# Optimization experiments

Measured on AMD Instinct MI355X. Metric: run time of the kernel, lower is better.

## Reference

```python
import jax, jax.numpy as jnp
import numpy as np

L, H, Wn, C = 2048, 768, 1024, 64


def setup_inputs() -> dict:
    key = jax.random.key(0)
    ks = jax.random.split(key, 12)
    s = 1.0 / np.sqrt(H)
    s3 = 1.0 / np.sqrt(3 * H)
    return {
        "tok_embs": jax.random.normal(ks[0], (L, H), jnp.float32),
        "wmask": jax.random.randint(ks[1], (L,), 0, Wn + 1),  # 1-indexed word positions, 0 = ignore
        "text_length": Wn,
        "label_embs": jax.random.normal(ks[2], (C, H), jnp.float32),
        "W_tok": jax.random.normal(ks[3], (H, 2 * H), jnp.float32) * s,
        "b_tok": jnp.zeros((2 * H,), jnp.float32),
        "W_lab": jax.random.normal(ks[4], (H, 2 * H), jnp.float32) * s,
        "b_lab": jnp.zeros((2 * H,), jnp.float32),
        "W1": jax.random.normal(ks[5], (3 * H, H), jnp.float32) * s3,
        "b1": jnp.zeros((H,), jnp.float32),
        "W2": jax.random.normal(ks[6], (H, 3), jnp.float32) * s,
        "b2": jnp.zeros((3,), jnp.float32),
    }


def reference(tok_embs, wmask, text_length, label_embs, W_tok, b_tok, W_lab, b_lab, W1, b1, W2, b2):
    Wd = text_length
    Hd = tok_embs.shape[-1]
    # --- word-level scatter pooling: we[wmask-1] = tok_embs where wmask > 0 ---
    # route masked-out tokens to a dummy row Wd, then drop it (jit-safe, no nonzero)
    tgt = jnp.where(wmask > 0, wmask - 1, Wd)
    we = jnp.zeros((Wd + 1, Hd), tok_embs.dtype).at[tgt].set(tok_embs)[:Wd]  # (W, H)
    # --- scorer ---
    t = (we @ W_tok + b_tok).reshape(Wd, 2, Hd)        # (W, 2, H)
    lb = (label_embs @ W_lab + b_lab).reshape(-1, 2, Hd)  # (C, 2, H)
    Cd = lb.shape[0]
    t0 = jnp.broadcast_to(t[:, None, 0, :], (Wd, Cd, Hd))
    l0 = jnp.broadcast_to(lb[None, :, 0, :], (Wd, Cd, Hd))
    prod = t[:, None, 1, :] * lb[None, :, 1, :]        # (W, C, H)
    cat = jnp.concatenate([t0, l0, prod], axis=-1)     # (W, C, 3H)
    h = jax.nn.relu(cat @ W1 + b1)                     # (W, C, H)
    scores = h @ W2 + b2                               # (W, C, 3)
    return scores
```

## Files before the change

kernel.cpp:

```cpp
#include <hip/hip_runtime.h>
#include <hip/hip_bf16.h>

static constexpr int Hd = 768;
static constexpr int H2 = 1536;
static constexpr int Cn = 64;

typedef __attribute__((ext_vector_type(8))) short short8;
typedef __attribute__((ext_vector_type(4))) float f32x4;
typedef unsigned short us;

__device__ inline unsigned int f2bf2(float a, float b) {
    __hip_bfloat162 h = __float22bfloat162_rn(float2{a, b});
    return *reinterpret_cast<unsigned int*>(&h);
}

__device__ inline void split1(float x, us& h, us& l) {
    __hip_bfloat16 hb = __float2bfloat16(x);
    float hf = __bfloat162float(hb);
    __hip_bfloat16 lb_ = __float2bfloat16(x - hf);
    h = *reinterpret_cast<us*>(&hb);
    l = *reinterpret_cast<us*>(&lb_);
}

__device__ inline us f2b(float x) {
    __hip_bfloat16 b = __float2bfloat16(x);
    return *reinterpret_cast<us*>(&b);
}

__device__ inline float b2f(us u) {
    __hip_bfloat16 b = *reinterpret_cast<__hip_bfloat16*>(&u);
    return __bfloat162float(b);
}

__device__ inline short8 bfmul8(short8 a, short8 b) {
    short8 r;
#pragma unroll
    for (int e = 0; e < 8; e += 2) {
        unsigned int p = f2bf2(b2f((us)a[e]) * b2f((us)b[e]),
                               b2f((us)a[e + 1]) * b2f((us)b[e + 1]));
        r[e] = (short)(p & 0xffff);
        r[e + 1] = (short)(p >> 16);
    }
    return r;
}

__device__ inline int swz(int row, int q) {
    return row * 32 + ((q ^ ((row >> 1) & 3)) << 3);
}

__device__ inline void gload16(const void* g, void* l) {
    __builtin_amdgcn_global_load_lds(
        (const __attribute__((address_space(1))) unsigned int*)g,
        (__attribute__((address_space(3))) unsigned int*)l, 16, 0, 0);
}

__global__ void k_init(int* widx, int Wd) {
    int i = blockIdx.x * 256 + threadIdx.x;
    if (i < Wd) widx[i] = -1;
}

__global__ void k_scatter(const int* __restrict__ wmask, int* widx, int L, int Wd) {
    int i = blockIdx.x * 256 + threadIdx.x;
    if (i < L) {
        int m = wmask[i];
        if (m > 0 && m <= Wd) atomicMax(&widx[m - 1], i);
    }
}

__global__ void k_build_we_split(const float4* __restrict__ tok, const int* __restrict__ widx,
                                 us* __restrict__ weh, us* __restrict__ wel, int Wd) {
    int i = blockIdx.x * 256 + threadIdx.x;
    if (i >= Wd * 192) return;
    int w = i / 192, c4 = i - w * 192;
    int idx = widx[w];
    float4 v = (idx >= 0) ? tok[idx * 192 + c4] : float4{0.f, 0.f, 0.f, 0.f};
    us hh[4], ll[4];
    split1(v.x, hh[0], ll[0]);
    split1(v.y, hh[1], ll[1]);
    split1(v.z, hh[2], ll[2]);
    split1(v.w, hh[3], ll[3]);
    size_t o = (size_t)w * Hd + c4 * 4;
    *(ushort4*)&weh[o] = ushort4{hh[0], hh[1], hh[2], hh[3]};
    *(ushort4*)&wel[o] = ushort4{ll[0], ll[1], ll[2], ll[3]};
}

struct TSArgs {
    const float* src[5];
    us* th[5];
    us* tl[5];
    int ld[5];
    int N[5];
};
__global__ __launch_bounds__(256)
void k_tsplit(TSArgs a) {
    __shared__ float tile[64][65];
    const int z = blockIdx.z;
    const int n0 = blockIdx.x * 64, k0 = blockIdx.y * 64;
    if (n0 >= a.N[z]) return;
    const float* W = a.src[z];
    const int ld = a.ld[z];
    for (int idx = threadIdx.x; idx < 4096; idx += 256) {
        int kk = idx >> 6, nn = idx & 63;
        tile[kk][nn] = W[(size_t)(k0 + kk) * ld + n0 + nn];
    }
    __syncthreads();
    us* Th = a.th[z];
    us* Tl = a.tl[z];
    for (int idx = threadIdx.x; idx < 4096; idx += 256) {
        int nn = idx >> 6, kk = idx & 63;
        us h, l;
        split1(tile[kk][nn], h, l);
        size_t o = (size_t)(n0 + nn) * Hd + k0 + kk;
        Th[o] = h;
        Tl[o] = l;
    }
}

__global__ __launch_bounds__(256)
void k_split(const float* __restrict__ x, int lda, int cols,
             us* __restrict__ h, us* __restrict__ l, int n4) {
    int i = blockIdx.x * 256 + threadIdx.x;
    if (i >= n4) return;
    int c4 = cols >> 2;
    int row = i / c4, cc = (i - row * c4) * 4;
    float4 v = *(const float4*)&x[(size_t)row * lda + cc];
    us hh[4], ll[4];
    split1(v.x, hh[0], ll[0]);
    split1(v.y, hh[1], ll[1]);
    split1(v.z, hh[2], ll[2]);
    split1(v.w, hh[3], ll[3]);
    size_t o = (size_t)row * cols + cc;
    *(ushort4*)&h[o] = ushort4{hh[0], hh[1], hh[2], hh[3]};
    *(ushort4*)&l[o] = ushort4{ll[0], ll[1], ll[2], ll[3]};
}

__global__ __launch_bounds__(256)
void k_gemm2(const us* __restrict__ Ah, const us* __restrict__ Al,
             const us* __restrict__ BhT, const us* __restrict__ BlT,
             float* __restrict__ Cpart, int M, int N, int K) {
    __shared__ __align__(16) us S[2][4][64 * 32];
    const int tid = threadIdx.x, wave = tid >> 6, lane = tid & 63;
    const int quad = lane >> 4, l15 = lane & 15;
    const int wm = wave & 1, wn = wave >> 1;
    const int m0 = blockIdx.y * 64, n0 = blockIdx.x * 64;
    const int Ks = K / gridDim.z, kbeg = blockIdx.z * Ks, kend = kbeg + Ks;
    float* C = Cpart + (size_t)blockIdx.z * M * N;

    const int srow = wave * 16 + (lane >> 2), soff = (lane & 3) * 8;
    const size_t gaB = (size_t)(m0 + srow) * K + soff;
    const size_t gbB = (size_t)(n0 + srow) * K + soff;
    const int lo = wave * 16 * 32;

    f32x4 acc[2][2];
#pragma unroll
    for (int a = 0; a < 2; ++a)
#pragma unroll
        for (int b = 0; b < 2; ++b) acc[a][b] = (f32x4){0.f, 0.f, 0.f, 0.f};

    auto stage = [&](int p, int k0) {
        gload16(Ah + gaB + k0, &S[p][0][lo]);
        gload16(Al + gaB + k0, &S[p][1][lo]);
        gload16(BhT + gbB + k0, &S[p][2][lo]);
        gload16(BlT + gbB + k0, &S[p][3][lo]);
    };

    int p = 0;
    stage(0, kbeg);
    for (int k0 = kbeg; k0 < kend; k0 += 32) {
        __syncthreads();
        if (k0 + 32 < kend) stage(p ^ 1, k0 + 32);
        short8 ah[2], al[2], bh[2], bl[2];
#pragma unroll
        for (int mt = 0; mt < 2; ++mt) {
            int off = (wm * 32 + mt * 16 + l15) * 32 + quad * 8;
            ah[mt] = *(const short8*)&S[p][0][off];
            al[mt] = *(const short8*)&S[p][1][off];
        }
#pragma unroll
        for (int nt = 0; nt < 2; ++nt) {
            int off = (wn * 32 + nt * 16 + l15) * 32 + quad * 8;
            bh[nt] = *(const short8*)&S[p][2][off];
            bl[nt] = *(const short8*)&S[p][3][off];
        }
#pragma unroll
        for (int mt = 0; mt < 2; ++mt)
#pragma unroll
            for (int nt = 0; nt < 2; ++nt) {
                acc[mt][nt] = __builtin_amdgcn_mfma_f32_16x16x32_bf16(al[mt], bh[nt], acc[mt][nt], 0, 0, 0);
                acc[mt][nt] = __builtin_amdgcn_mfma_f32_16x16x32_bf16(ah[mt], bl[nt], acc[mt][nt], 0, 0, 0);
                acc[mt][nt] = __builtin_amdgcn_mfma_f32_16x16x32_bf16(ah[mt], bh[nt], acc[mt][nt], 0, 0, 0);
            }
        p ^= 1;
    }
#pragma unroll
    for (int mt = 0; mt < 2; ++mt)
#pragma unroll
        for (int nt = 0; nt < 2; ++nt) {
            int col = n0 + wn * 32 + nt * 16 + l15;
#pragma unroll
            for (int reg = 0; reg < 4; ++reg) {
                int row = m0 + wm * 32 + mt * 16 + quad * 4 + reg;
                C[(size_t)row * N + col] = acc[mt][nt][reg];
            }
        }
}

__global__ __launch_bounds__(256)
void k_gemm3(const us* __restrict__ Ah, const us* __restrict__ Al,
             const us* __restrict__ BhT, const us* __restrict__ BlT,
             const float* __restrict__ bias, float* __restrict__ outF,
             us* __restrict__ sh, us* __restrict__ sl, us* __restrict__ bh16,
             int scols, int N, int K) {
    __shared__ __align__(16) us S[2][4][64 * 32];
    const int tid = threadIdx.x, wave = tid >> 6, lane = tid & 63;
    const int quad = lane >> 4, l15 = lane & 15;
    const int wm = wave & 1, wn = wave >> 1;
    const int m0 = blockIdx.y * 64, n0 = blockIdx.x * 64;

    const int srow = wave * 16 + (lane >> 2), soff = (lane & 3) * 8;
    const size_t gaB = (size_t)(m0 + srow) * K + soff;
    const size_t gbB = (size_t)(n0 + srow) * K + soff;
    const int lo = wave * 16 * 32;

    f32x4 acc[2][2];
#pragma unroll
    for (int a = 0; a < 2; ++a)
#pragma unroll
        for (int b = 0; b < 2; ++b) acc[a][b] = (f32x4){0.f, 0.f, 0.f, 0.f};

    auto stage = [&](int p, int k0) {
        gload16(Ah + gaB + k0, &S[p][0][lo]);
        gload16(Al + gaB + k0, &S[p][1][lo]);
        gload16(BhT + gbB + k0, &S[p][2][lo]);
        gload16(BlT + gbB + k0, &S[p][3][lo]);
    };

    int p = 0;
    stage(0, 0);
    for (int k0 = 0; k0 < K; k0 += 32) {
        __syncthreads();
        if (k0 + 32 < K) stage(p ^ 1, k0 + 32);
        short8 ah[2], al[2], bh[2], bl[2];
#pragma unroll
        for (int mt = 0; mt < 2; ++mt) {
            int off = (wm * 32 + mt * 16 + l15) * 32 + quad * 8;
            ah[mt] = *(const short8*)&S[p][0][off];
            al[mt] = *(const short8*)&S[p][1][off];
        }
#pragma unroll
        for (int nt = 0; nt < 2; ++nt) {
            int off = (wn * 32 + nt * 16 + l15) * 32 + quad * 8;
            bh[nt] = *(const short8*)&S[p][2][off];
            bl[nt] = *(const short8*)&S[p][3][off];
        }
#pragma unroll
        for (int mt = 0; mt < 2; ++mt)
#pragma unroll
            for (int nt = 0; nt < 2; ++nt) {
                acc[mt][nt] = __builtin_amdgcn_mfma_f32_16x16x32_bf16(al[mt], bh[nt], acc[mt][nt], 0, 0, 0);
                acc[mt][nt] = __builtin_amdgcn_mfma_f32_16x16x32_bf16(ah[mt], bl[nt], acc[mt][nt], 0, 0, 0);
                acc[mt][nt] = __builtin_amdgcn_mfma_f32_16x16x32_bf16(ah[mt], bh[nt], acc[mt][nt], 0, 0, 0);
            }
        p ^= 1;
    }
#pragma unroll
    for (int mt = 0; mt < 2; ++mt)
#pragma unroll
        for (int nt = 0; nt < 2; ++nt) {
            int col = n0 + wn * 32 + nt * 16 + l15;
            float bb = bias ? bias[col] : 0.f;
#pragma unroll
            for (int reg = 0; reg < 4; ++reg) {
                int row = m0 + wm * 32 + mt * 16 + quad * 4 + reg;
                float v = acc[mt][nt][reg] + bb;
                if (outF) outF[(size_t)row * N + col] = v;
                if (sh) {
                    if (col < scols) {
                        us h, l;
                        split1(v, h, l);
                        size_t o = (size_t)row * scols + col;
                        sh[o] = h;
                        sl[o] = l;
                    } else if (bh16) {
                        bh16[(size_t)row * scols + (col - scols)] = f2b(v);
                    }
                }
            }
        }
}

__global__ __launch_bounds__(256)
void k_reduce(const float* __restrict__ part, int S, int MN, int N,
              const float* __restrict__ bias, float* __restrict__ outF,
              us* __restrict__ sh, us* __restrict__ sl, int scols,
              us* __restrict__ bh16) {
    int i = blockIdx.x * 256 + threadIdx.x;
    if (i >= MN) return;
    float v = 0.f;
    for (int s = 0; s < S; ++s) v += part[(size_t)s * MN + i];
    int row = i / N, col = i - row * N;
    if (bias) v += bias[col];
    if (outF) outF[i] = v;
    if (col < scols) {
        if (sh) {
            us h, l;
            split1(v, h, l);
            size_t o = (size_t)row * scols + col;
            sh[o] = h;
            sl[o] = l;
        }
    } else if (bh16) {
        bh16[(size_t)row * scols + (col - scols)] = f2b(v);
    }
}

__global__ __launch_bounds__(256, 3)
void k_mfma7(const us* __restrict__ t1b,
             const us* __restrict__ W1ct,
             const us* __restrict__ lb1b,
             const float* __restrict__ Aw,
             const float* __restrict__ Bc,
             const float* __restrict__ W2,
             float* __restrict__ scr) {
    __shared__ __align__(16) us As[2][128 * 32];
    __shared__ __align__(16) us Bs[2][128 * 32];
    __shared__ float sred[128 * 3];

    const int tid = threadIdx.x, wave = tid >> 6, lane = tid & 63;
    const int quad = lane >> 4, l15 = lane & 15;
    const int wm = wave & 1, wn = wave >> 1;

    const int b = blockIdx.x;
    const int xcd = b & 7, slot = b >> 3;
    const int cgrp = slot / 48, tt = slot % 48;
    const int my = tt / 6, jx = tt - my * 6;
    const int c = cgrp * 8 + xcd;
    const int jt = jx * 128, m0 = my * 128;

    for (int i = tid; i < 128 * 3; i += 256) sred[i] = 0.f;

    const int aro = tid >> 1;
    const int qb = (tid & 1) * 2;
    const int kbase = qb * 8;
    const us* gA = W1ct + (size_t)(jt + aro) * Hd + kbase;
    const us* gL = lb1b + (size_t)c * Hd + kbase;
    const us* gB = t1b + (size_t)(m0 + aro) * Hd + kbase;
    const int w0 = swz(aro, qb), w1 = swz(aro, qb + 1);

    f32x4 acc[4][4];
#pragma unroll
    for (int mt = 0; mt < 4; ++mt)
#pragma unroll
        for (int nt = 0; nt < 4; ++nt) acc[mt][nt] = (f32x4){0.f, 0.f, 0.f, 0.f};

    short8 aw0l, aw0h, al0l, al0h, b0l, b0h;
    short8 aw1l, aw1h, al1l, al1h, b1l, b1h;

    aw0l = *(const short8*)(gA + 0);  aw0h = *(const short8*)(gA + 8);
    al0l = *(const short8*)(gL + 0);  al0h = *(const short8*)(gL + 8);
    b0l  = *(const short8*)(gB + 0);  b0h  = *(const short8*)(gB + 8);
    aw1l = *(const short8*)(gA + 32); aw1h = *(const short8*)(gA + 40);
    al1l = *(const short8*)(gL + 32); al1h = *(const short8*)(gL + 40);
    b1l  = *(const short8*)(gB + 32); b1h  = *(const short8*)(gB + 40);
    *(short8*)&As[0][w0] = bfmul8(aw0l, al0l);
    *(short8*)&As[0][w1] = bfmul8(aw0h, al0h);
    *(short8*)&Bs[0][w0] = b0l;
    *(short8*)&Bs[0][w1] = b0h;
    __syncthreads();

    for (int k = 0; k < Hd; k += 64) {
        {
            short8 af[4], bf[4];
#pragma unroll
            for (int mt = 0; mt < 4; ++mt)
                af[mt] = *(const short8*)&As[0][swz(wm * 64 + mt * 16 + l15, quad)];
#pragma unroll
            for (int nt = 0; nt < 4; ++nt)
                bf[nt] = *(const short8*)&Bs[0][swz(wn * 64 + nt * 16 + l15, quad)];
            if (k + 64 < Hd) {
                aw0l = *(const short8*)(gA + k + 64); aw0h = *(const short8*)(gA + k + 72);
                al0l = *(const short8*)(gL + k + 64); al0h = *(const short8*)(gL + k + 72);
                b0l  = *(const short8*)(gB + k + 64); b0h  = *(const short8*)(gB + k + 72);
            }
#pragma unroll
            for (int mt = 0; mt < 4; ++mt)
#pragma unroll
                for (int nt = 0; nt < 4; ++nt)
                    acc[mt][nt] = __builtin_amdgcn_mfma_f32_16x16x32_bf16(
                        af[mt], bf[nt], acc[mt][nt], 0, 0, 0);
            *(short8*)&As[1][w0] = bfmul8(aw1l, al1l);
            *(short8*)&As[1][w1] = bfmul8(aw1h, al1h);
            *(short8*)&Bs[1][w0] = b1l;
            *(short8*)&Bs[1][w1] = b1h;
            __syncthreads();
        }
        {
            short8 af[4], bf[4];
#pragma unroll
            for (int mt = 0; mt < 4; ++mt)
                af[mt] = *(const short8*)&As[1][swz(wm * 64 + mt * 16 + l15, quad)];
#pragma unroll
            for (int nt = 0; nt < 4; ++nt)
                bf[nt] = *(const short8*)&Bs[1][swz(wn * 64 + nt * 16 + l15, quad)];
            if (k + 96 < Hd) {
                aw1l = *(const short8*)(gA + k + 96); aw1h = *(const short8*)(gA + k + 104);
                al1l = *(const short8*)(gL + k + 96); al1h = *(const short8*)(gL + k + 104);
                b1l  = *(const short8*)(gB + k + 96); b1h  = *(const short8*)(gB + k + 104);
            }
#pragma unroll
            for (int mt = 0; mt < 4; ++mt)
#pragma unroll
                for (int nt = 0; nt < 4; ++nt)
                    acc[mt][nt] = __builtin_amdgcn_mfma_f32_16x16x32_bf16(
                        af[mt], bf[nt], acc[mt][nt], 0, 0, 0);
            if (k + 64 < Hd) {
                *(short8*)&As[0][w0] = bfmul8(aw0l, al0l);
                *(short8*)&As[0][w1] = bfmul8(aw0h, al0h);
                *(short8*)&Bs[0][w0] = b0l;
                *(short8*)&Bs[0][w1] = b0h;
                __syncthreads();
            }
        }
    }

    float bcv[4][4], w2v[4][4][3];
#pragma unroll
    for (int mt = 0; mt < 4; ++mt) {
        const int jb = jt + wm * 64 + mt * 16 + quad * 4;
        float4 b4 = *(const float4*)&Bc[(size_t)c * Hd + jb];
        bcv[mt][0] = b4.x; bcv[mt][1] = b4.y; bcv[mt][2] = b4.z; bcv[mt][3] = b4.w;
#pragma unroll
        for (int reg = 0; reg < 4; ++reg)
#pragma unroll
            for (int r = 0; r < 3; ++r) w2v[mt][reg][r] = W2[(jb + reg) * 3 + r];
    }
#pragma unroll
    for (int nt = 0; nt < 4; ++nt) {
        const int w = m0 + wn * 64 + nt * 16 + l15;
        const float* awp = Aw + (size_t)w * Hd + jt + wm * 64;
        float s0 = 0.f, s1 = 0.f, s2 = 0.f;
#pragma unroll
        for (int mt = 0; mt < 4; ++mt) {
            float4 a4 = *(const float4*)&awp[mt * 16 + quad * 4];
            float av[4] = {a4.x, a4.y, a4.z, a4.w};
#pragma unroll
            for (int reg = 0; reg < 4; ++reg) {
                float h = acc[mt][nt][reg] + av[reg] + bcv[mt][reg];
                h = h > 0.f ? h : 0.f;
                s0 += h * w2v[mt][reg][0];
                s1 += h * w2v[mt][reg][1];
                s2 += h * w2v[mt][reg][2];
            }
        }
        s0 += __shfl_xor(s0, 16); s0 += __shfl_xor(s0, 32);
        s1 += __shfl_xor(s1, 16); s1 += __shfl_xor(s1, 32);
        s2 += __shfl_xor(s2, 16); s2 += __shfl_xor(s2, 32);
        if (quad == 0) {
            const int wl = wn * 64 + nt * 16 + l15;
            atomicAdd(&sred[wl * 3 + 0], s0);
            atomicAdd(&sred[wl * 3 + 1], s1);
            atomicAdd(&sred[wl * 3 + 2], s2);
        }
    }
    __syncthreads();
    float* slab = scr + ((size_t)jx * 1024 * Cn + (size_t)m0 * Cn + c) * 3;
    for (int i = tid; i < 128 * 3; i += 256) {
        int wl = i / 3, r = i - wl * 3;
        slab[(size_t)wl * Cn * 3 + r] = sred[i];
    }
}

__global__ __launch_bounds__(256)
void k_scores(const float* __restrict__ scr, const float* __restrict__ b2,
              float* __restrict__ out, int n) {
    int i = blockIdx.x * 256 + threadIdx.x;
    if (i >= n) return;
    float v = b2[i % 3];
#pragma unroll
    for (int s = 0; s < 6; ++s) v += scr[(size_t)s * n + i];
    out[i] = v;
}

extern "C" void kernel_launch(void* const* d_in, const int* in_sizes, int n_in,
                              void* d_out, int out_size, void* d_ws, size_t ws_size,
                              hipStream_t stream) {
    const float* tok    = (const float*)d_in[0];
    const int*   wmask  = (const int*)d_in[1];
    const float* labe   = (const float*)d_in[3];
    const float* W_tok  = (const float*)d_in[4];
    const float* b_tok  = (const float*)d_in[5];
    const float* W_lab  = (const float*)d_in[6];
    const float* b_lab  = (const float*)d_in[7];
    const float* W1     = (const float*)d_in[8];
    const float* b1     = (const float*)d_in[9];
    const float* W2     = (const float*)d_in[10];
    const float* b2     = (const float*)d_in[11];
    float* out = (float*)d_out;

    const int L  = in_sizes[1];
    const int Wd = out_size / (Cn * 3);

    char* ws = (char*)d_ws;
    size_t off = 0;
    auto alloc = [&](size_t bytes) { char* p = ws + off; off += (bytes + 255) & ~(size_t)255; return p; };
    int*   widx  = (int*)alloc(4096);
    float* Abuf  = (float*)alloc((size_t)Wd * Hd * 4);
    float* Bbuf  = (float*)alloc((size_t)Cn * Hd * 4);
    us* W1ct  = (us*)alloc((size_t)Hd * Hd * 2);
    us* W1cl  = (us*)alloc((size_t)Hd * Hd * 2);
    us* t1b   = (us*)alloc((size_t)Wd * Hd * 2);
    us* lb1b  = (us*)alloc((size_t)Cn * Hd * 2);
    float* scr = (float*)alloc((size_t)6 * Wd * Cn * 3 * 4);
    us* WtTh  = (us*)alloc((size_t)H2 * Hd * 2);
    us* WtTl  = (us*)alloc((size_t)H2 * Hd * 2);
    us* WlTh  = (us*)alloc((size_t)H2 * Hd * 2);
    us* WlTl  = (us*)alloc((size_t)H2 * Hd * 2);
    us* W1aTh = (us*)alloc((size_t)Hd * Hd * 2);
    us* W1aTl = (us*)alloc((size_t)Hd * Hd * 2);
    us* W1bTh = (us*)alloc((size_t)Hd * Hd * 2);
    us* W1bTl = (us*)alloc((size_t)Hd * Hd * 2);
    us* weh   = (us*)alloc((size_t)Wd * Hd * 2);
    us* wel   = (us*)alloc((size_t)Wd * Hd * 2);
    us* lah   = (us*)alloc((size_t)Cn * Hd * 2);
    us* lal   = (us*)alloc((size_t)Cn * Hd * 2);
    us* t0h   = (us*)alloc((size_t)Wd * Hd * 2);
    us* t0l   = (us*)alloc((size_t)Wd * Hd * 2);
    us* lb0h  = (us*)alloc((size_t)Cn * Hd * 2);
    us* lb0l  = (us*)alloc((size_t)Cn * Hd * 2);
    float* part = (float*)alloc((size_t)8 * Cn * H2 * 4);

    k_init<<<(Wd + 255) / 256, 256, 0, stream>>>(widx, Wd);
    k_scatter<<<(L + 255) / 256, 256, 0, stream>>>(wmask, widx, L, Wd);
    k_build_we_split<<<(Wd * 192 + 255) / 256, 256, 0, stream>>>((const float4*)tok, widx, weh, wel, Wd);

    TSArgs ts;
    ts.src[0] = W_tok;  ts.th[0] = WtTh;  ts.tl[0] = WtTl;  ts.ld[0] = H2; ts.N[0] = H2;
    ts.src[1] = W_lab;  ts.th[1] = WlTh;  ts.tl[1] = WlTl;  ts.ld[1] = H2; ts.N[1] = H2;
    ts.src[2] = W1;                         ts.th[2] = W1aTh; ts.tl[2] = W1aTl; ts.ld[2] = Hd; ts.N[2] = Hd;
    ts.src[3] = W1 + (size_t)Hd * Hd;       ts.th[3] = W1bTh; ts.tl[3] = W1bTl; ts.ld[3] = Hd; ts.N[3] = Hd;
    ts.src[4] = W1 + (size_t)2 * Hd * Hd;   ts.th[4] = W1ct;  ts.tl[4] = W1cl;  ts.ld[4] = Hd; ts.N[4] = Hd;
    k_tsplit<<<dim3(H2 / 64, Hd / 64, 5), 256, 0, stream>>>(ts);

    k_split<<<(Cn * Hd / 4 + 255) / 256, 256, 0, stream>>>(labe, Hd, Hd, lah, lal, Cn * Hd / 4);

    k_gemm3<<<dim3(H2 / 64, Wd / 64), 256, 0, stream>>>(weh, wel, WtTh, WtTl, b_tok,
                                                        nullptr, t0h, t0l, t1b, Hd, H2, Hd);

    k_gemm2<<<dim3(H2 / 64, 1, 8), 256, 0, stream>>>(lah, lal, WlTh, WlTl, part, Cn, H2, Hd);
    k_reduce<<<(Cn * H2 + 255) / 256, 256, 0, stream>>>(part, 8, Cn * H2, H2, b_lab, nullptr, lb0h, lb0l, Hd, lb1b);

    k_gemm3<<<dim3(Hd / 64, Wd / 64), 256, 0, stream>>>(t0h, t0l, W1aTh, W1aTl, nullptr,
                                                        Abuf, nullptr, nullptr, nullptr, 0, Hd, Hd);

    k_gemm2<<<dim3(Hd / 64, 1, 8), 256, 0, stream>>>(lb0h, lb0l, W1bTh, W1bTl, part, Cn, Hd, Hd);
    k_reduce<<<(Cn * Hd + 255) / 256, 256, 0, stream>>>(part, 8, Cn * Hd, Hd, b1, Bbuf, nullptr, nullptr, Hd, nullptr);

    k_mfma7<<<3072, 256, 0, stream>>>(t1b, W1ct, lb1b, Abuf, Bbuf, W2, scr);

    k_scores<<<(Wd * Cn * 3 + 255) / 256, 256, 0, stream>>>(scr, b2, out, Wd * Cn * 3);
}
```

Measured before the change: 276.1 us.

## Double word tile to 256 and load B fragments directly from global into registers

The main MFMA kernel now covers 256 word rows per block instead of 128, doubling the accumulator tile to 4x8 per wave and halving the grid. The B operand (t1b) is no longer staged through shared memory. Each wave loads its MFMA fragments straight from global memory into registers and double-buffers them. This removes the LDS writes, reads and their share of the barriers, and reuses each A tile across twice as many words. In exchange, register pressure rises (occupancy bound lowered to 2), global loads become strided per row, and fewer blocks may hurt load balance.

```diff
diff --git a/kernel.cpp b/kernel.cpp
--- a/kernel.cpp
+++ b/kernel.cpp
@@ -314,8 +314,8 @@
     }
 }
 
-__global__ __launch_bounds__(256, 3)
-void k_mfma7(const us* __restrict__ t1b,
+__global__ __launch_bounds__(256, 2)
+void k_mfma8(const us* __restrict__ t1b,
              const us* __restrict__ W1ct,
              const us* __restrict__ lb1b,
              const float* __restrict__ Aw,
@@ -323,8 +323,7 @@
              const float* __restrict__ W2,
              float* __restrict__ scr) {
     __shared__ __align__(16) us As[2][128 * 32];
-    __shared__ __align__(16) us Bs[2][128 * 32];
-    __shared__ float sred[128 * 3];
+    __shared__ float sred[256 * 3];
 
     const int tid = threadIdx.x, wave = tid >> 6, lane = tid & 63;
     const int quad = lane >> 4, l15 = lane & 15;
@@ -332,92 +331,91 @@
 
     const int b = blockIdx.x;
     const int xcd = b & 7, slot = b >> 3;
-    const int cgrp = slot / 48, tt = slot % 48;
+    const int cgrp = slot / 24, tt = slot % 24;
     const int my = tt / 6, jx = tt - my * 6;
     const int c = cgrp * 8 + xcd;
-    const int jt = jx * 128, m0 = my * 128;
-
-    for (int i = tid; i < 128 * 3; i += 256) sred[i] = 0.f;
+    const int jt = jx * 128, m0 = my * 256;
+
+    for (int i = tid; i < 256 * 3; i += 256) sred[i] = 0.f;
 
     const int aro = tid >> 1;
     const int qb = (tid & 1) * 2;
     const int kbase = qb * 8;
     const us* gA = W1ct + (size_t)(jt + aro) * Hd + kbase;
     const us* gL = lb1b + (size_t)c * Hd + kbase;
-    const us* gB = t1b + (size_t)(m0 + aro) * Hd + kbase;
     const int w0 = swz(aro, qb), w1 = swz(aro, qb + 1);
 
-    f32x4 acc[4][4];
+    const us* gB = t1b + (size_t)(m0 + wn * 128 + l15) * Hd + quad * 8;
+
+    f32x4 acc[4][8];
 #pragma unroll
     for (int mt = 0; mt < 4; ++mt)
 #pragma unroll
-        for (int nt = 0; nt < 4; ++nt) acc[mt][nt] = (f32x4){0.f, 0.f, 0.f, 0.f};
-
-    short8 aw0l, aw0h, al0l, al0h, b0l, b0h;
-    short8 aw1l, aw1h, al1l, al1h, b1l, b1h;
+        for (int nt = 0; nt < 8; ++nt) acc[mt][nt] = (f32x4){0.f, 0.f, 0.f, 0.f};
+
+    short8 aw0l, aw0h, aw1l, aw1h, all_, alh_;
+    short8 bcur[8], bnxt[8];
 
     aw0l = *(const short8*)(gA + 0);  aw0h = *(const short8*)(gA + 8);
-    al0l = *(const short8*)(gL + 0);  al0h = *(const short8*)(gL + 8);
-    b0l  = *(const short8*)(gB + 0);  b0h  = *(const short8*)(gB + 8);
     aw1l = *(const short8*)(gA + 32); aw1h = *(const short8*)(gA + 40);
-    al1l = *(const short8*)(gL + 32); al1h = *(const short8*)(gL + 40);
-    b1l  = *(const short8*)(gB + 32); b1h  = *(const short8*)(gB + 40);
-    *(short8*)&As[0][w0] = bfmul8(aw0l, al0l);
-    *(short8*)&As[0][w1] = bfmul8(aw0h, al0h);
-    *(short8*)&Bs[0][w0] = b0l;
-    *(short8*)&Bs[0][w1] = b0h;
+    all_ = *(const short8*)(gL + 0);  alh_ = *(const short8*)(gL + 8);
+#pragma unroll
+    for (int nt = 0; nt < 8; ++nt)
+        bcur[nt] = *(const short8*)(gB + (size_t)nt * 16 * Hd);
+    *(short8*)&As[0][w0] = bfmul8(aw0l, all_);
+    *(short8*)&As[0][w1] = bfmul8(aw0h, alh_);
     __syncthreads();
 
     for (int k = 0; k < Hd; k += 64) {
         {
-            short8 af[4], bf[4];
+            short8 af[4];
 #pragma unroll
             for (int mt = 0; mt < 4; ++mt)
                 af[mt] = *(const short8*)&As[0][swz(wm * 64 + mt * 16 + l15, quad)];
-#pragma unroll
-            for (int nt = 0; nt < 4; ++nt)
-                bf[nt] = *(const short8*)&Bs[0][swz(wn * 64 + nt * 16 + l15, quad)];
             if (k + 64 < Hd) {
-                aw0l = *(const short8*)(gA + k + 64); aw0h = *(const short8*)(gA + k + 72);
-                al0l = *(const short8*)(gL + k + 64); al0h = *(const short8*)(gL + k + 72);
-                b0l  = *(const short8*)(gB + k + 64); b0h  = *(const short8*)(gB + k + 72);
-            }
+                aw0l = *(const short8*)(gA + k + 64);
+                aw0h = *(const short8*)(gA + k + 72);
+            }
+#pragma unroll
+            for (int nt = 0; nt < 8; ++nt)
+                bnxt[nt] = *(const short8*)(gB + (size_t)nt * 16 * Hd + k + 32);
 #pragma unroll
             for (int mt = 0; mt < 4; ++mt)
 #pragma unroll
-                for (int nt = 0; nt < 4; ++nt)
+                for (int nt = 0; nt < 8; ++nt)
                     acc[mt][nt] = __builtin_amdgcn_mfma_f32_16x16x32_bf16(
-                        af[mt], bf[nt], acc[mt][nt], 0, 0, 0);
-            *(short8*)&As[1][w0] = bfmul8(aw1l, al1l);
-            *(short8*)&As[1][w1] = bfmul8(aw1h, al1h);
-            *(short8*)&Bs[1][w0] = b1l;
-            *(short8*)&Bs[1][w1] = b1h;
+                        af[mt], bcur[nt], acc[mt][nt], 0, 0, 0);
+            all_ = *(const short8*)(gL + k + 32);
+            alh_ = *(const short8*)(gL + k + 40);
+            *(short8*)&As[1][w0] = bfmul8(aw1l, all_);
+            *(short8*)&As[1][w1] = bfmul8(aw1h, alh_);
             __syncthreads();
         }
         {
-            short8 af[4], bf[4];
+            short8 af[4];
 #pragma unroll
             for (int mt = 0; mt < 4; ++mt)
                 af[mt] = *(const short8*)&As[1][swz(wm * 64 + mt * 16 + l15, quad)];
-#pragma unroll
-            for (int nt = 0; nt < 4; ++nt)
-                bf[nt] = *(const short8*)&Bs[1][swz(wn * 64 + nt * 16 + l15, quad)];
             if (k + 96 < Hd) {
-                aw1l = *(const short8*)(gA + k + 96); aw1h = *(const short8*)(gA + k + 104);
-                al1l = *(const short8*)(gL + k + 96); al1h = *(const short8*)(gL + k + 104);
-                b1l  = *(const short8*)(gB + k + 96); b1h  = *(const short8*)(gB + k + 104);
+                aw1l = *(const short8*)(gA + k + 96);
+                aw1h = *(const short8*)(gA + k + 104);
+            }
+            if (k + 64 < Hd) {
+#pragma unroll
+                for (int nt = 0; nt < 8; ++nt)
+                    bcur[nt] = *(const short8*)(gB + (size_t)nt * 16 * Hd + k + 64);
             }
 #pragma unroll
             for (int mt = 0; mt < 4; ++mt)
 #pragma unroll
-                for (int nt = 0; nt < 4; ++nt)
+                for (int nt = 0; nt < 8; ++nt)
                     acc[mt][nt] = __builtin_amdgcn_mfma_f32_16x16x32_bf16(
-                        af[mt], bf[nt], acc[mt][nt], 0, 0, 0);
+                        af[mt], bnxt[nt], acc[mt][nt], 0, 0, 0);
             if (k + 64 < Hd) {
-                *(short8*)&As[0][w0] = bfmul8(aw0l, al0l);
-                *(short8*)&As[0][w1] = bfmul8(aw0h, al0h);
-                *(short8*)&Bs[0][w0] = b0l;
-                *(short8*)&Bs[0][w1] = b0h;
+                all_ = *(const short8*)(gL + k + 64);
+                alh_ = *(const short8*)(gL + k + 72);
+                *(short8*)&As[0][w0] = bfmul8(aw0l, all_);
+                *(short8*)&As[0][w1] = bfmul8(aw0h, alh_);
                 __syncthreads();
             }
         }
@@ -435,8 +433,8 @@
             for (int r = 0; r < 3; ++r) w2v[mt][reg][r] = W2[(jb + reg) * 3 + r];
     }
 #pragma unroll
-    for (int nt = 0; nt < 4; ++nt) {
-        const int w = m0 + wn * 64 + nt * 16 + l15;
+    for (int nt = 0; nt < 8; ++nt) {
+        const int w = m0 + wn * 128 + nt * 16 + l15;
         const float* awp = Aw + (size_t)w * Hd + jt + wm * 64;
         float s0 = 0.f, s1 = 0.f, s2 = 0.f;
 #pragma unroll
@@ -456,7 +454,7 @@
         s1 += __shfl_xor(s1, 16); s1 += __shfl_xor(s1, 32);
         s2 += __shfl_xor(s2, 16); s2 += __shfl_xor(s2, 32);
         if (quad == 0) {
-            const int wl = wn * 64 + nt * 16 + l15;
+            const int wl = wn * 128 + nt * 16 + l15;
             atomicAdd(&sred[wl * 3 + 0], s0);
             atomicAdd(&sred[wl * 3 + 1], s1);
             atomicAdd(&sred[wl * 3 + 2], s2);
@@ -464,7 +462,7 @@
     }
     __syncthreads();
     float* slab = scr + ((size_t)jx * 1024 * Cn + (size_t)m0 * Cn + c) * 3;
-    for (int i = tid; i < 128 * 3; i += 256) {
+    for (int i = tid; i < 256 * 3; i += 256) {
         int wl = i / 3, r = i - wl * 3;
         slab[(size_t)wl * Cn * 3 + r] = sred[i];
     }
@@ -555,7 +553,7 @@
     k_gemm2<<<dim3(Hd / 64, 1, 8), 256, 0, stream>>>(lb0h, lb0l, W1bTh, W1bTl, part, Cn, Hd, Hd);
     k_reduce<<<(Cn * Hd + 255) / 256, 256, 0, stream>>>(part, 8, Cn * Hd, Hd, b1, Bbuf, nullptr, nullptr, Hd, nullptr);
 
-    k_mfma7<<<3072, 256, 0, stream>>>(t1b, W1ct, lb1b, Abuf, Bbuf, W2, scr);
+    k_mfma8<<<1536, 256, 0, stream>>>(t1b, W1ct, lb1b, Abuf, Bbuf, W2, scr);
 
     k_scores<<<(Wd * Cn * 3 + 255) / 256, 256, 0, stream>>>(scr, b2, out, Wd * Cn * 3);
 }
```

Result: slower. 341.5 us (+23.7%).
